# Performance work log

Measured on AMD Instinct MI355X. Metric: run time of the kernel, lower is better.

Reference implementation:

```python
import jax, jax.numpy as jnp
import numpy as np

WS = 7            # window size
HEADS = 4
DIM = 128         # hidden_dim
HEAD_DIM = 128    # wrapper passes head_dim=hidden_dim (faithful to source)
INNER = HEADS * HEAD_DIM   # 512
MLP = 4 * DIM
PATCH = 4
DISP = WS // 2
NEG = -1e9


def _ln(x, g, b, eps=1e-5):
    m = jnp.mean(x, -1, keepdims=True)
    v = jnp.mean((x - m) ** 2, -1, keepdims=True)
    return (x - m) * jax.lax.rsqrt(v + eps) * g + b


_coords = np.stack(np.meshgrid(np.arange(WS), np.arange(WS), indexing='ij'), -1).reshape(-1, 2)
REL_IDX = jnp.asarray(_coords[None] - _coords[:, None] + WS - 1)  # (ws^2, ws^2, 2)


def _build_masks():
    n = WS * WS
    ul = np.zeros((n, n), np.float32)
    ul[-DISP * WS:, : -DISP * WS] = NEG
    ul[: -DISP * WS, -DISP * WS:] = NEG
    lr = np.zeros((WS, WS, WS, WS), np.float32)
    lr[:, -DISP:, :, : -DISP] = NEG
    lr[:, : -DISP, :, -DISP:] = NEG
    return jnp.asarray(ul), jnp.asarray(lr.reshape(n, n))

UL_MASK, LR_MASK = _build_masks()


def _win_attn(x, w_qkv, pos, w_o, b_o, shifted):
    b, H, W, _ = x.shape
    if shifted:
        x = jnp.roll(x, (-DISP, -DISP), axis=(1, 2))
    nh, nw = H // WS, W // WS
    qkv = x @ w_qkv  # (b, H, W, 3*INNER)

    def to_win(t):  # -> (b, heads, n_windows, ws*ws, head_dim)
        t = t.reshape(b, nh, WS, nw, WS, HEADS, HEAD_DIM)
        return t.transpose(0, 5, 1, 3, 2, 4, 6).reshape(b, HEADS, nh * nw, WS * WS, HEAD_DIM)

    q, k, v = map(to_win, jnp.split(qkv, 3, axis=-1))
    dots = jnp.einsum('bhwid,bhwjd->bhwij', q, k) * (HEAD_DIM ** -0.5)
    dots = dots + pos[REL_IDX[..., 0], REL_IDX[..., 1]]  # shared across heads (berniwal)
    if shifted:
        dots = dots.at[:, :, -nw:].add(UL_MASK)
        dots = dots.at[:, :, nw - 1::nw].add(LR_MASK)
    attn = jax.nn.softmax(dots, axis=-1)
    out = jnp.einsum('bhwij,bhwjd->bhwid', attn, v)
    out = out.reshape(b, HEADS, nh, nw, WS, WS, HEAD_DIM).transpose(0, 2, 4, 3, 5, 1, 6)
    out = out.reshape(b, H, W, INNER) @ w_o + b_o
    if shifted:
        out = jnp.roll(out, (DISP, DISP), axis=(1, 2))
    return out


def _block(x, ga1, be1, w_qkv, pos, w_o, b_o, ga2, be2, w1, b1, w2, b2, shifted):
    x = x + _win_attn(_ln(x, ga1, be1), w_qkv, pos, w_o, b_o, shifted)
    h = jax.nn.gelu(_ln(x, ga2, be2) @ w1 + b1, approximate=False) @ w2 + b2
    return x + h


def _patch_embed(x, w, b):  # Unfold(patch) + Linear, channel-major feature order
    B, C, H, W = x.shape
    nh, nw = H // PATCH, W // PATCH
    x = x.reshape(B, C, nh, PATCH, nw, PATCH).transpose(0, 2, 4, 1, 3, 5)
    return x.reshape(B, nh, nw, C * PATCH * PATCH) @ w + b


def setup_inputs() -> dict:
    key = jax.random.key(0)
    ks = iter(jax.random.split(key, 48))

    def nrm(shape, s=0.02):
        return jax.random.normal(next(ks), shape, dtype=jnp.float32) * s

    inp = {'x': jax.random.normal(next(ks), (32, 3, 224, 224), dtype=jnp.float32)}
    inp['w_pe'] = nrm((3 * PATCH * PATCH, DIM))
    inp['b_pe'] = jnp.zeros((DIM,), jnp.float32)
    for s in ('a', 'b'):
        inp['ga1_' + s] = jnp.ones((DIM,), jnp.float32)
        inp['be1_' + s] = jnp.zeros((DIM,), jnp.float32)
        inp['w_qkv_' + s] = nrm((DIM, 3 * INNER))
        inp['pos_' + s] = nrm((2 * WS - 1, 2 * WS - 1), 1.0)
        inp['w_o_' + s] = nrm((INNER, DIM))
        inp['b_o_' + s] = jnp.zeros((DIM,), jnp.float32)
        inp['ga2_' + s] = jnp.ones((DIM,), jnp.float32)
        inp['be2_' + s] = jnp.zeros((DIM,), jnp.float32)
        inp['w_m1_' + s] = nrm((DIM, MLP))
        inp['b_m1_' + s] = jnp.zeros((MLP,), jnp.float32)
        inp['w_m2_' + s] = nrm((MLP, DIM))
        inp['b_m2_' + s] = jnp.zeros((DIM,), jnp.float32)
    return inp


def reference(x, w_pe, b_pe,
              ga1_a, be1_a, w_qkv_a, pos_a, w_o_a, b_o_a, ga2_a, be2_a, w_m1_a, b_m1_a, w_m2_a, b_m2_a,
              ga1_b, be1_b, w_qkv_b, pos_b, w_o_b, b_o_b, ga2_b, be2_b, w_m1_b, b_m1_b, w_m2_b, b_m2_b):
    h = _patch_embed(x, w_pe, b_pe)  # (B, 56, 56, DIM)
    h = _block(h, ga1_a, be1_a, w_qkv_a, pos_a, w_o_a, b_o_a, ga2_a, be2_a, w_m1_a, b_m1_a, w_m2_a, b_m2_a, False)
    h = _block(h, ga1_b, be1_b, w_qkv_b, pos_b, w_o_b, b_o_b, ga2_b, be2_b, w_m1_b, b_m1_b, w_m2_b, b_m2_b, True)
    return h
```

## Files before the change

### kernel.cpp

```cpp
#include <hip/hip_runtime.h>

typedef __attribute__((ext_vector_type(8))) short bf16x8;
typedef __attribute__((ext_vector_type(4))) short bf16x4;
typedef __attribute__((ext_vector_type(4))) float f32x4;
typedef __attribute__((ext_vector_type(2))) unsigned u32x2;

#define MFMA16(a, b, c) __builtin_amdgcn_mfma_f32_16x16x32_bf16(a, b, c, 0, 0, 0)

static __device__ __forceinline__ short f2bf(float f) {
    union { float f; unsigned u; } x; x.f = f;
    unsigned r = x.u + 0x7FFFu + ((x.u >> 16) & 1u);
    return (short)(r >> 16);
}

static __device__ __forceinline__ unsigned cvtpk(float lo, float hi) {
    unsigned r;
    asm("v_cvt_pk_bf16_f32 %0, %1, %2" : "=v"(r) : "v"(lo), "v"(hi));
    return r;
}

static __device__ __forceinline__ void gload16(const void* g, void* l) {
    __builtin_amdgcn_global_load_lds((const __attribute__((address_space(1))) void*)g,
                                     (__attribute__((address_space(3))) void*)l, 16, 0, 0);
}

static __device__ __forceinline__ float gelu(float t) {
    return 0.5f * t * (1.f + erff(t * 0.70710678118f));
}

__global__ void wconv_kernel(const float* __restrict__ i_qkv, const float* __restrict__ i_o,
                             const float* __restrict__ i_m1, const float* __restrict__ i_m2,
                             short* __restrict__ wqkv, short* __restrict__ wo,
                             short* __restrict__ wm1, short* __restrict__ wm2) {
    int idx = blockIdx.x * 256 + threadIdx.x;
    if (idx < 196608) {
        int k = idx & 127, n = idx >> 7;
        wqkv[idx] = f2bf(i_qkv[k * 1536 + n]);
    } else if (idx < 262144) {
        int l = idx - 196608; int k = l & 511, n = l >> 9;
        wo[l] = f2bf(i_o[k * 128 + n]);
    } else if (idx < 327680) {
        int l = idx - 262144; int k = l & 127, n = l >> 7;
        wm1[l] = f2bf(i_m1[k * 512 + n]);
    } else {
        int l = idx - 327680; int k = l & 511, n = l >> 9;
        wm2[l] = f2bf(i_m2[k * 128 + n]);
    }
}

__global__ void tabgen_kernel(const float* __restrict__ pos_a, const float* __restrict__ pos_b,
                              float* __restrict__ tab) {
    int v = blockIdx.x;
    const float* pos = (v == 0) ? pos_a : pos_b;
    for (int e = threadIdx.x; e < 4096; e += 256) {
        int row = e >> 6, key = e & 63;
        float val;
        if (key >= 49) val = -1e9f;
        else if (row >= 49) val = 0.f;
        else {
            int qi = row / 7, qj = row - qi * 7, ki = key / 7, kj = key - ki * 7;
            val = pos[(ki - qi + 6) * 13 + (kj - qj + 6)];
            if (v >= 1) {
                bool wh7 = (v - 1) & 2, ww7 = (v - 1) & 1;
                if (wh7 && ((qi >= 4) != (ki >= 4))) val += -1e9f;
                if (ww7 && ((qj >= 4) != (kj >= 4))) val += -1e9f;
            }
        }
        tab[v * 4096 + e] = val;
    }
}

__global__ __launch_bounds__(256) void patchln_kernel(const float* __restrict__ x,
                                                      const float* __restrict__ w,
                                                      const float* __restrict__ bias,
                                                      const float* __restrict__ g,
                                                      const float* __restrict__ bta,
                                                      float* __restrict__ out,
                                                      short* __restrict__ xn) {
    __shared__ float s_in[2][48];
    __shared__ float red[2][2][2];
    const int tid = threadIdx.x;
    const int half = tid >> 7, c = tid & 127;
    const int winh = (tid >> 6) & 1, lane = tid & 63;
    const int t = blockIdx.x * 2 + half;
    const int b = t / 3136, rem = t - b * 3136;
    const int hp = rem / 56, wp = rem - hp * 56;
    if (c < 48) {
        int cin = c >> 4, py = (c >> 2) & 3, px = c & 3;
        s_in[half][c] = x[((size_t)(b * 3 + cin) * 224 + hp * 4 + py) * 224 + wp * 4 + px];
    }
    __syncthreads();
    float acc = bias[c];
#pragma unroll
    for (int k = 0; k < 48; ++k) acc += s_in[half][k] * w[k * 128 + c];
    out[(size_t)t * 128 + c] = acc;
    float s1 = acc, s2 = acc * acc;
#pragma unroll
    for (int o = 32; o > 0; o >>= 1) { s1 += __shfl_xor(s1, o); s2 += __shfl_xor(s2, o); }
    if (lane == 0) { red[half][winh][0] = s1; red[half][winh][1] = s2; }
    __syncthreads();
    s1 = red[half][0][0] + red[half][1][0];
    s2 = red[half][0][1] + red[half][1][1];
    float mean = s1 * (1.f / 128.f);
    float var = s2 * (1.f / 128.f) - mean * mean;
    float rstd = rsqrtf(var + 1e-5f);
    xn[(size_t)t * 128 + c] = f2bf((acc - mean) * rstd * g[c] + bta[c]);
}

template <int SHIFTED>
__global__ __launch_bounds__(256, 3) void attn_kernel(const short* __restrict__ xn,
                                                      const short* __restrict__ wqkvT,
                                                      const float* __restrict__ tab,
                                                      const short* __restrict__ zpad,
                                                      short* __restrict__ aout) {
    __shared__ short smem[24576];
    short* s_x = smem;
    short* s_q = smem + 8192;
    short* s_k = smem + 16384;
    short* s_vT = smem + 8192;
    short* s_p = smem + 16384;

    const int tid = threadIdx.x;
    const int wid = tid >> 6, lane = tid & 63;
    const int l15 = lane & 15, l4 = lane >> 4, klo = l4 * 8;
    const int bid = blockIdx.x;
    const int win = bid & 63, head = (bid >> 6) & 3, b = bid >> 8;
    const int wh = win >> 3, ww = win & 7;

#pragma unroll
    for (int it = 0; it < 4; ++it) {
        int slot = it * 256 + tid;
        int row = slot >> 4, scol = slot & 15;
        int colb = (scol * 16) ^ ((row & 7) << 4);
        const char* g;
        if (row < 49) {
            int wi = (row * 37) >> 8, wj = row - wi * 7;
            int hh = wh * 7 + wi, wp = ww * 7 + wj;
            if (SHIFTED) { hh += 3; if (hh >= 56) hh -= 56; wp += 3; if (wp >= 56) wp -= 56; }
            int t = (b * 56 + hh) * 56 + wp;
            g = (const char*)(xn + (size_t)t * 128) + colb;
        } else {
            g = (const char*)zpad + colb;
        }
        gload16(g, (char*)smem + (it * 256 + wid * 64) * 16);
    }
    __syncthreads();

    const f32x4 zero4 = {0.f, 0.f, 0.f, 0.f};

    {
        const short* Wq = wqkvT + (size_t)(head * 128) * 128;
        const short* Wk = wqkvT + (size_t)(512 + head * 128) * 128;
        f32x4 aq[2][4], ak[2][4];
#pragma unroll
        for (int mw = 0; mw < 2; ++mw)
#pragma unroll
            for (int j = 0; j < 4; ++j) { aq[mw][j] = zero4; ak[mw][j] = zero4; }
#pragma unroll
        for (int k0 = 0; k0 < 4; ++k0) {
            bf16x8 bx[4], awq[2], awk[2];
#pragma unroll
            for (int j = 0; j < 4; ++j) {
                int row = j * 16 + l15;
                bx[j] = *(const bf16x8*)((const char*)s_x + row * 256 + ((k0 * 64 + l4 * 16) ^ ((row & 7) << 4)));
            }
#pragma unroll
            for (int mw = 0; mw < 2; ++mw) {
                awq[mw] = *(const bf16x8*)(Wq + (size_t)(wid * 32 + mw * 16 + l15) * 128 + k0 * 32 + klo);
                awk[mw] = *(const bf16x8*)(Wk + (size_t)(wid * 32 + mw * 16 + l15) * 128 + k0 * 32 + klo);
            }
            __builtin_amdgcn_s_setprio(1);
#pragma unroll
            for (int mw = 0; mw < 2; ++mw)
#pragma unroll
                for (int j = 0; j < 4; ++j) {
                    aq[mw][j] = MFMA16(awq[mw], bx[j], aq[mw][j]);
                    ak[mw][j] = MFMA16(awk[mw], bx[j], ak[mw][j]);
                }
            __builtin_amdgcn_s_setprio(0);
        }
#pragma unroll
        for (int mw = 0; mw < 2; ++mw)
#pragma unroll
            for (int j = 0; j < 4; ++j) {
                u32x2 pq = { cvtpk(aq[mw][j][0], aq[mw][j][1]), cvtpk(aq[mw][j][2], aq[mw][j][3]) };
                u32x2 pk = { cvtpk(ak[mw][j][0], ak[mw][j][1]), cvtpk(ak[mw][j][2], ak[mw][j][3]) };
                int row = j * 16 + l15;
                int colb = (wid * 64 + mw * 32 + l4 * 8) ^ ((row & 7) << 4);
                *(u32x2*)((char*)s_q + row * 256 + colb) = pq;
                *(u32x2*)((char*)s_k + row * 256 + colb) = pk;
            }
    }
    __syncthreads();

    const int qrow = wid * 16 + l15;
    f32x4 dt[4];
#pragma unroll
    for (int m = 0; m < 4; ++m) dt[m] = zero4;
#pragma unroll
    for (int k0 = 0; k0 < 4; ++k0) {
        bf16x8 bq = *(const bf16x8*)((const char*)s_q + qrow * 256 + ((k0 * 64 + l4 * 16) ^ ((qrow & 7) << 4)));
        __builtin_amdgcn_s_setprio(1);
#pragma unroll
        for (int m = 0; m < 4; ++m) {
            int krow = m * 16 + l15;
            bf16x8 akf = *(const bf16x8*)((const char*)s_k + krow * 256 + ((k0 * 64 + l4 * 16) ^ ((krow & 7) << 4)));
            dt[m] = MFMA16(akf, bq, dt[m]);
        }
        __builtin_amdgcn_s_setprio(0);
    }
    __syncthreads();

    const int variant = SHIFTED ? (1 + ((wh == 7) ? 2 : 0) + ((ww == 7) ? 1 : 0)) : 0;
    const float* tv = tab + variant * 4096 + qrow * 64;
    const float SC = 0.08838834764831845f;
    float p[4][4];
    float mx = -3.0e38f;
#pragma unroll
    for (int m = 0; m < 4; ++m) {
        f32x4 tb = *(const f32x4*)(tv + m * 16 + l4 * 4);
#pragma unroll
        for (int r = 0; r < 4; ++r) {
            float d = dt[m][r] * SC + tb[r];
            p[m][r] = d;
            mx = fmaxf(mx, d);
        }
    }
    mx = fmaxf(mx, __shfl_xor(mx, 16));
    mx = fmaxf(mx, __shfl_xor(mx, 32));
    float sum = 0.f;
#pragma unroll
    for (int m = 0; m < 4; ++m)
#pragma unroll
        for (int r = 0; r < 4; ++r) { p[m][r] = __expf(p[m][r] - mx); sum += p[m][r]; }
    sum += __shfl_xor(sum, 16);
    sum += __shfl_xor(sum, 32);
    float inv = 1.f / sum;
#pragma unroll
    for (int m = 0; m < 4; ++m) {
        u32x2 pv = { cvtpk(p[m][0] * inv, p[m][1] * inv), cvtpk(p[m][2] * inv, p[m][3] * inv) };
        *(u32x2*)((char*)s_p + qrow * 128 + ((m * 32 + l4 * 8) ^ ((qrow & 7) << 4))) = pv;
    }

    {
        const short* Wv = wqkvT + (size_t)(1024 + head * 128) * 128;
        f32x4 acc[4][2];
#pragma unroll
        for (int m = 0; m < 4; ++m)
#pragma unroll
            for (int n = 0; n < 2; ++n) acc[m][n] = zero4;
#pragma unroll
        for (int k0 = 0; k0 < 4; ++k0) {
            bf16x8 ax[4], bw[2];
#pragma unroll
            for (int m = 0; m < 4; ++m) {
                int row = m * 16 + l15;
                ax[m] = *(const bf16x8*)((const char*)s_x + row * 256 + ((k0 * 64 + l4 * 16) ^ ((row & 7) << 4)));
            }
#pragma unroll
            for (int n = 0; n < 2; ++n)
                bw[n] = *(const bf16x8*)(Wv + (size_t)(wid * 32 + n * 16 + l15) * 128 + k0 * 32 + klo);
            __builtin_amdgcn_s_setprio(1);
#pragma unroll
            for (int m = 0; m < 4; ++m)
#pragma unroll
                for (int n = 0; n < 2; ++n) acc[m][n] = MFMA16(ax[m], bw[n], acc[m][n]);
            __builtin_amdgcn_s_setprio(0);
        }
#pragma unroll
        for (int m = 0; m < 4; ++m)
#pragma unroll
            for (int n = 0; n < 2; ++n) {
                u32x2 pv = { cvtpk(acc[m][n][0], acc[m][n][1]), cvtpk(acc[m][n][2], acc[m][n][3]) };
                int hd = wid * 32 + n * 16 + l15;
                *(u32x2*)((char*)s_vT + hd * 128 + ((m * 32 + l4 * 8) ^ ((hd & 7) << 4))) = pv;
            }
    }
    __syncthreads();

    f32x4 o[4][2];
#pragma unroll
    for (int m = 0; m < 4; ++m)
#pragma unroll
        for (int n = 0; n < 2; ++n) o[m][n] = zero4;
#pragma unroll
    for (int k0 = 0; k0 < 2; ++k0) {
        bf16x8 ap[4], bv[2];
#pragma unroll
        for (int m = 0; m < 4; ++m) {
            int row = m * 16 + l15;
            ap[m] = *(const bf16x8*)((const char*)s_p + row * 128 + ((k0 * 64 + l4 * 16) ^ ((row & 7) << 4)));
        }
#pragma unroll
        for (int n = 0; n < 2; ++n) {
            int hd = wid * 32 + n * 16 + l15;
            bv[n] = *(const bf16x8*)((const char*)s_vT + hd * 128 + ((k0 * 64 + l4 * 16) ^ ((hd & 7) << 4)));
        }
        __builtin_amdgcn_s_setprio(1);
#pragma unroll
        for (int m = 0; m < 4; ++m)
#pragma unroll
            for (int n = 0; n < 2; ++n) o[m][n] = MFMA16(ap[m], bv[n], o[m][n]);
        __builtin_amdgcn_s_setprio(0);
    }
#pragma unroll
    for (int m = 0; m < 4; ++m) {
#pragma unroll
        for (int r = 0; r < 4; ++r) {
            int rl = m * 16 + l4 * 4 + r;
            if (rl < 49) {
                int wi = (rl * 37) >> 8, wj = rl - wi * 7;
                int hh = wh * 7 + wi, wp = ww * 7 + wj;
                if (SHIFTED) { hh += 3; if (hh >= 56) hh -= 56; wp += 3; if (wp >= 56) wp -= 56; }
                size_t t = (size_t)(b * 56 + hh) * 56 + wp;
                aout[t * 512 + head * 128 + wid * 32 + l15] = f2bf(o[m][0][r]);
                aout[t * 512 + head * 128 + wid * 32 + 16 + l15] = f2bf(o[m][1][r]);
            }
        }
    }
}

__global__ __launch_bounds__(256, 2) void projmlp_kernel(const short* __restrict__ A,
                                                         const short* __restrict__ woT,
                                                         const short* __restrict__ wm1T,
                                                         const float* __restrict__ b_o,
                                                         const float* __restrict__ ga2,
                                                         const float* __restrict__ be2,
                                                         const float* __restrict__ b1,
                                                         float* __restrict__ outf,
                                                         short* __restrict__ hid) {
    __shared__ char smem[65536];
    float* red = (float*)(smem + 32768);

    const int tid = threadIdx.x, wid = tid >> 6, lane = tid & 63;
    const int wr = wid >> 1, wc = wid & 1;
    const int l15 = lane & 15, l4 = lane >> 4;
    const int m0 = blockIdx.x * 128;

    auto stage = [&](int kc, int bi) {
#pragma unroll
        for (int it = 0; it < 4; ++it) {
            int slot = it * 256 + tid;
            int row = slot >> 3, scol = slot & 7;
            int colb = (scol * 16) ^ ((row & 7) << 4);
            gload16((const char*)(A + (size_t)(m0 + row) * 512 + kc * 64) + colb,
                    (char*)smem + bi * 32768 + (it * 256 + wid * 64) * 16);
        }
#pragma unroll
        for (int it = 0; it < 4; ++it) {
            int slot = it * 256 + tid;
            int row = slot >> 3, scol = slot & 7;
            int colb = (scol * 16) ^ ((row & 7) << 4);
            gload16((const char*)(woT + (size_t)row * 512 + kc * 64) + colb,
                    (char*)smem + bi * 32768 + 16384 + (it * 256 + wid * 64) * 16);
        }
    };

    const f32x4 zero4 = {0.f, 0.f, 0.f, 0.f};
    f32x4 acc[4][4];
#pragma unroll
    for (int nf = 0; nf < 4; ++nf)
#pragma unroll
        for (int tm = 0; tm < 4; ++tm) acc[nf][tm] = zero4;

    stage(0, 0);
    __syncthreads();
#pragma unroll
    for (int kc = 0; kc < 8; ++kc) {
        if (kc + 1 < 8) stage(kc + 1, (kc + 1) & 1);
        const char* bufA = (const char*)smem + (kc & 1) * 32768;
        const char* bufB = bufA + 16384;
#pragma unroll
        for (int ks = 0; ks < 2; ++ks) {
            bf16x8 a[4], bfr[4];
#pragma unroll
            for (int tm = 0; tm < 4; ++tm) {
                int row = wr * 64 + tm * 16 + l15;
                a[tm] = *(const bf16x8*)(bufA + row * 128 + ((ks * 64 + l4 * 16) ^ ((row & 7) << 4)));
            }
#pragma unroll
            for (int nf = 0; nf < 4; ++nf) {
                int row = wc * 64 + nf * 16 + l15;
                bfr[nf] = *(const bf16x8*)(bufB + row * 128 + ((ks * 64 + l4 * 16) ^ ((row & 7) << 4)));
            }
            __builtin_amdgcn_s_setprio(1);
#pragma unroll
            for (int nf = 0; nf < 4; ++nf)
#pragma unroll
                for (int tm = 0; tm < 4; ++tm) acc[nf][tm] = MFMA16(bfr[nf], a[tm], acc[nf][tm]);
            __builtin_amdgcn_s_setprio(0);
        }
        __syncthreads();
    }

    f32x4 bv4[4];
#pragma unroll
    for (int nf = 0; nf < 4; ++nf)
        bv4[nf] = *(const f32x4*)(b_o + wc * 64 + nf * 16 + l4 * 4);

    float s1[4], s2[4];
#pragma unroll
    for (int tm = 0; tm < 4; ++tm) {
        int row = m0 + wr * 64 + tm * 16 + l15;
        float a1 = 0.f, a2 = 0.f;
#pragma unroll
        for (int nf = 0; nf < 4; ++nf) {
            f32x4 rs = *(const f32x4*)(outf + (size_t)row * 128 + wc * 64 + nf * 16 + l4 * 4);
#pragma unroll
            for (int r = 0; r < 4; ++r) {
                float v = acc[nf][tm][r] + bv4[nf][r] + rs[r];
                acc[nf][tm][r] = v;
                a1 += v; a2 += v * v;
            }
        }
        s1[tm] = a1; s2[tm] = a2;
    }
#pragma unroll
    for (int tm = 0; tm < 4; ++tm) {
        s1[tm] += __shfl_xor(s1[tm], 16); s1[tm] += __shfl_xor(s1[tm], 32);
        s2[tm] += __shfl_xor(s2[tm], 16); s2[tm] += __shfl_xor(s2[tm], 32);
    }
    if (l4 == 0) {
#pragma unroll
        for (int tm = 0; tm < 4; ++tm) {
            int lrow = wr * 64 + tm * 16 + l15;
            red[lrow * 4 + wc * 2] = s1[tm];
            red[lrow * 4 + wc * 2 + 1] = s2[tm];
        }
    }
    __syncthreads();

    float mean[4], rstd[4];
#pragma unroll
    for (int tm = 0; tm < 4; ++tm) {
        int lrow = wr * 64 + tm * 16 + l15;
        f32x4 rd = *(const f32x4*)(red + lrow * 4);
        float t1 = rd[0] + rd[2], t2 = rd[1] + rd[3];
        mean[tm] = t1 * (1.f / 128.f);
        float var = t2 * (1.f / 128.f) - mean[tm] * mean[tm];
        rstd[tm] = rsqrtf(var + 1e-5f);
    }
    __syncthreads();

#pragma unroll
    for (int tm = 0; tm < 4; ++tm) {
        int lrow = wr * 64 + tm * 16 + l15;
        int row = m0 + lrow;
#pragma unroll
        for (int nf = 0; nf < 4; ++nf) {
            int col0 = wc * 64 + nf * 16 + l4 * 4;
            *(f32x4*)(outf + (size_t)row * 128 + col0) = acc[nf][tm];
            f32x4 gg = *(const f32x4*)(ga2 + col0);
            f32x4 bb = *(const f32x4*)(be2 + col0);
            float w0 = (acc[nf][tm][0] - mean[tm]) * rstd[tm] * gg[0] + bb[0];
            float w1 = (acc[nf][tm][1] - mean[tm]) * rstd[tm] * gg[1] + bb[1];
            float w2 = (acc[nf][tm][2] - mean[tm]) * rstd[tm] * gg[2] + bb[2];
            float w3 = (acc[nf][tm][3] - mean[tm]) * rstd[tm] * gg[3] + bb[3];
            u32x2 pb = { cvtpk(w0, w1), cvtpk(w2, w3) };
            *(u32x2*)((char*)smem + lrow * 256 + ((col0 * 2) ^ ((lrow & 7) << 4))) = pb;
        }
    }
    __syncthreads();

    for (int hc = 0; hc < 4; ++hc) {
#pragma unroll
        for (int it = 0; it < 8; ++it) {
            int slot = it * 256 + tid;
            int row = slot >> 4, scol = slot & 15;
            int colb = (scol * 16) ^ ((row & 7) << 4);
            gload16((const char*)(wm1T + (size_t)(hc * 128 + row) * 128) + colb,
                    (char*)smem + 32768 + (it * 256 + wid * 64) * 16);
        }
        __syncthreads();

#pragma unroll
        for (int nf = 0; nf < 4; ++nf)
#pragma unroll
            for (int tm = 0; tm < 4; ++tm) acc[nf][tm] = zero4;
#pragma unroll
        for (int ks = 0; ks < 4; ++ks) {
            bf16x8 a[4], bfr[4];
#pragma unroll
            for (int tm = 0; tm < 4; ++tm) {
                int row = wr * 64 + tm * 16 + l15;
                a[tm] = *(const bf16x8*)((const char*)smem + row * 256 + ((ks * 64 + l4 * 16) ^ ((row & 7) << 4)));
            }
#pragma unroll
            for (int nf = 0; nf < 4; ++nf) {
                int hrow = wc * 64 + nf * 16 + l15;
                bfr[nf] = *(const bf16x8*)((const char*)smem + 32768 + hrow * 256 + ((ks * 64 + l4 * 16) ^ ((hrow & 7) << 4)));
            }
            __builtin_amdgcn_s_setprio(1);
#pragma unroll
            for (int nf = 0; nf < 4; ++nf)
#pragma unroll
                for (int tm = 0; tm < 4; ++tm) acc[nf][tm] = MFMA16(bfr[nf], a[tm], acc[nf][tm]);
            __builtin_amdgcn_s_setprio(0);
        }

        f32x4 b14[4];
#pragma unroll
        for (int nf = 0; nf < 4; ++nf)
            b14[nf] = *(const f32x4*)(b1 + hc * 128 + wc * 64 + nf * 16 + l4 * 4);
#pragma unroll
        for (int tm = 0; tm < 4; ++tm) {
            int row = m0 + wr * 64 + tm * 16 + l15;
#pragma unroll
            for (int nf = 0; nf < 4; ++nf) {
                float v0 = gelu(acc[nf][tm][0] + b14[nf][0]);
                float v1 = gelu(acc[nf][tm][1] + b14[nf][1]);
                float v2 = gelu(acc[nf][tm][2] + b14[nf][2]);
                float v3 = gelu(acc[nf][tm][3] + b14[nf][3]);
                u32x2 pv = { cvtpk(v0, v1), cvtpk(v2, v3) };
                *(u32x2*)(hid + (size_t)row * 512 + hc * 128 + wc * 64 + nf * 16 + l4 * 4) = pv;
            }
        }
        __syncthreads();
    }
}

template <int MODE>
__global__ __launch_bounds__(256, 2) void gemm4_kernel(const short* __restrict__ A,
                                                       const short* __restrict__ BT,
                                                       const float* __restrict__ bias,
                                                       const float* __restrict__ g,
                                                       const float* __restrict__ bta,
                                                       float* __restrict__ outf,
                                                       short* __restrict__ outb) {
    __shared__ char smem[65536];
    float* red = (float*)smem;

    const int tid = threadIdx.x, wid = tid >> 6, lane = tid & 63;
    const int wr = wid >> 1, wc = wid & 1;
    const int l15 = lane & 15, l4 = lane >> 4;
    const int m0 = blockIdx.x * 128;

    auto stage = [&](int kc, int bi) {
#pragma unroll
        for (int it = 0; it < 4; ++it) {
            int slot = it * 256 + tid;
            int row = slot >> 3, scol = slot & 7;
            int colb = (scol * 16) ^ ((row & 7) << 4);
            gload16((const char*)(A + (size_t)(m0 + row) * 512 + kc * 64) + colb,
                    (char*)smem + bi * 32768 + (it * 256 + wid * 64) * 16);
        }
#pragma unroll
        for (int it = 0; it < 4; ++it) {
            int slot = it * 256 + tid;
            int row = slot >> 3, scol = slot & 7;
            int colb = (scol * 16) ^ ((row & 7) << 4);
            gload16((const char*)(BT + (size_t)row * 512 + kc * 64) + colb,
                    (char*)smem + bi * 32768 + 16384 + (it * 256 + wid * 64) * 16);
        }
    };

    const f32x4 zero4 = {0.f, 0.f, 0.f, 0.f};
    f32x4 acc[4][4];
#pragma unroll
    for (int nf = 0; nf < 4; ++nf)
#pragma unroll
        for (int tm = 0; tm < 4; ++tm) acc[nf][tm] = zero4;

    stage(0, 0);
    __syncthreads();
#pragma unroll
    for (int kc = 0; kc < 8; ++kc) {
        if (kc + 1 < 8) stage(kc + 1, (kc + 1) & 1);
        const char* bufA = (const char*)smem + (kc & 1) * 32768;
        const char* bufB = bufA + 16384;
#pragma unroll
        for (int ks = 0; ks < 2; ++ks) {
            bf16x8 a[4], bfr[4];
#pragma unroll
            for (int tm = 0; tm < 4; ++tm) {
                int row = wr * 64 + tm * 16 + l15;
                a[tm] = *(const bf16x8*)(bufA + row * 128 + ((ks * 64 + l4 * 16) ^ ((row & 7) << 4)));
            }
#pragma unroll
            for (int nf = 0; nf < 4; ++nf) {
                int row = wc * 64 + nf * 16 + l15;
                bfr[nf] = *(const bf16x8*)(bufB + row * 128 + ((ks * 64 + l4 * 16) ^ ((row & 7) << 4)));
            }
            __builtin_amdgcn_s_setprio(1);
#pragma unroll
            for (int nf = 0; nf < 4; ++nf)
#pragma unroll
                for (int tm = 0; tm < 4; ++tm) acc[nf][tm] = MFMA16(bfr[nf], a[tm], acc[nf][tm]);
            __builtin_amdgcn_s_setprio(0);
        }
        __syncthreads();
    }

    f32x4 bv4[4];
#pragma unroll
    for (int nf = 0; nf < 4; ++nf)
        bv4[nf] = *(const f32x4*)(bias + wc * 64 + nf * 16 + l4 * 4);

    float s1[4], s2[4];
#pragma unroll
    for (int tm = 0; tm < 4; ++tm) {
        int row = m0 + wr * 64 + tm * 16 + l15;
        float a1 = 0.f, a2 = 0.f;
#pragma unroll
        for (int nf = 0; nf < 4; ++nf) {
            f32x4 rs = *(const f32x4*)(outf + (size_t)row * 128 + wc * 64 + nf * 16 + l4 * 4);
#pragma unroll
            for (int r = 0; r < 4; ++r) {
                float v = acc[nf][tm][r] + bv4[nf][r] + rs[r];
                acc[nf][tm][r] = v;
                a1 += v; a2 += v * v;
            }
        }
        s1[tm] = a1; s2[tm] = a2;
    }

    if (MODE == 1) {
#pragma unroll
        for (int tm = 0; tm < 4; ++tm) {
            s1[tm] += __shfl_xor(s1[tm], 16); s1[tm] += __shfl_xor(s1[tm], 32);
            s2[tm] += __shfl_xor(s2[tm], 16); s2[tm] += __shfl_xor(s2[tm], 32);
        }
        if (l4 == 0) {
#pragma unroll
            for (int tm = 0; tm < 4; ++tm) {
                int lrow = wr * 64 + tm * 16 + l15;
                red[lrow * 4 + wc * 2] = s1[tm];
                red[lrow * 4 + wc * 2 + 1] = s2[tm];
            }
        }
        __syncthreads();
    }

#pragma unroll
    for (int tm = 0; tm < 4; ++tm) {
        int lrow = wr * 64 + tm * 16 + l15;
        int row = m0 + lrow;
        float mean = 0.f, rstd = 0.f;
        if (MODE == 1) {
            f32x4 rd = *(const f32x4*)(red + lrow * 4);
            float t1 = rd[0] + rd[2], t2 = rd[1] + rd[3];
            mean = t1 * (1.f / 128.f);
            float var = t2 * (1.f / 128.f) - mean * mean;
            rstd = rsqrtf(var + 1e-5f);
        }
#pragma unroll
        for (int nf = 0; nf < 4; ++nf) {
            int col0 = wc * 64 + nf * 16 + l4 * 4;
            *(f32x4*)(outf + (size_t)row * 128 + col0) = acc[nf][tm];
            if (MODE == 1) {
                f32x4 gg = *(const f32x4*)(g + col0);
                f32x4 bb = *(const f32x4*)(bta + col0);
                float w0 = (acc[nf][tm][0] - mean) * rstd * gg[0] + bb[0];
                float w1 = (acc[nf][tm][1] - mean) * rstd * gg[1] + bb[1];
                float w2 = (acc[nf][tm][2] - mean) * rstd * gg[2] + bb[2];
                float w3 = (acc[nf][tm][3] - mean) * rstd * gg[3] + bb[3];
                u32x2 pb = { cvtpk(w0, w1), cvtpk(w2, w3) };
                *(u32x2*)(outb + (size_t)row * 128 + col0) = pb;
            }
        }
    }
}

extern "C" void kernel_launch(void* const* d_in, const int* in_sizes, int n_in,
                              void* d_out, int out_size, void* d_ws, size_t ws_size,
                              hipStream_t stream) {
    const float* x = (const float*)d_in[0];
    const float* w_pe = (const float*)d_in[1];
    const float* b_pe = (const float*)d_in[2];
    const float* P[24];
    for (int i = 0; i < 24; ++i) P[i] = (const float*)d_in[3 + i];

    float* out = (float*)d_out;
    const size_t TOK = 100352;

    short* xn = (short*)d_ws;
    short* abuf = xn + TOK * 128;
    short* wqkv = abuf + TOK * 512;
    short* wo = wqkv + 196608;
    short* wm1 = wo + 65536;
    short* wm2 = wm1 + 65536;
    float* tab = (float*)(wm2 + 65536);
    short* zpad = (short*)(tab + 5 * 4096);

    hipMemsetAsync(zpad, 0, 256, stream);
    tabgen_kernel<<<5, 256, 0, stream>>>(P[3], P[15], tab);

    patchln_kernel<<<50176, 256, 0, stream>>>(x, w_pe, b_pe, P[0], P[1], out, xn);

    for (int s = 0; s < 2; ++s) {
        wconv_kernel<<<1536, 256, 0, stream>>>(P[s * 12 + 2], P[s * 12 + 4], P[s * 12 + 8], P[s * 12 + 10],
                                               wqkv, wo, wm1, wm2);

        if (s == 0)
            attn_kernel<0><<<8192, 256, 0, stream>>>(xn, wqkv, tab, zpad, abuf);
        else
            attn_kernel<1><<<8192, 256, 0, stream>>>(xn, wqkv, tab, zpad, abuf);

        projmlp_kernel<<<784, 256, 0, stream>>>(
            abuf, wo, wm1, P[s * 12 + 5], P[s * 12 + 6], P[s * 12 + 7], P[s * 12 + 9], out, abuf);

        if (s == 0)
            gemm4_kernel<1><<<784, 256, 0, stream>>>(
                abuf, wm2, P[11], P[12], P[13], out, xn);
        else
            gemm4_kernel<2><<<784, 256, 0, stream>>>(
                abuf, wm2, P[23], nullptr, nullptr, out, nullptr);
    }
}
```

Measured before the change: 594.3 us.

## Fold Wq·Wkᵀ into a per-head matrix so attention skips the K projection

A new per-head 128x128 matrix M = Wq_h·Wk_hᵀ·scale is precomputed from the weights in fp32 and stored in bf16. The attention kernel now computes T = X·M and forms the scores as T·Xᵀ directly against the staged input, so it no longer projects K and no longer applies the scale per element. The V projection moves into the first GEMM phase alongside T, which removes one staged-input pass, and the shared-memory regions are reassigned. The cost is a small extra weight-precompute kernel per block, plus different rounding because M is formed in fp32 but stored in bf16. The MLP accumulator is renamed, which may affect register allocation.

```diff
diff --git a/kernel.cpp b/kernel.cpp
--- a/kernel.cpp
+++ b/kernel.cpp
@@ -46,6 +46,20 @@
         int l = idx - 327680; int k = l & 511, n = l >> 9;
         wm2[l] = f2bf(i_m2[k * 128 + n]);
     }
+}
+
+__global__ __launch_bounds__(128) void mtgen_kernel(const float* __restrict__ wqkv,
+                                                    short* __restrict__ mt) {
+    const int h = blockIdx.x >> 7, e = blockIdx.x & 127;
+    __shared__ float s_wk[128];
+    const int d = threadIdx.x;
+    s_wk[d] = wqkv[(size_t)e * 1536 + 512 + h * 128 + d];
+    __syncthreads();
+    const float* wq = wqkv + (size_t)d * 1536 + h * 128;
+    float acc = 0.f;
+#pragma unroll
+    for (int o = 0; o < 128; ++o) acc += wq[o] * s_wk[o];
+    mt[(size_t)(h * 128 + e) * 128 + d] = f2bf(acc * 0.08838834764831845f);
 }
 
 __global__ void tabgen_kernel(const float* __restrict__ pos_a, const float* __restrict__ pos_b,
@@ -110,15 +124,15 @@
 template <int SHIFTED>
 __global__ __launch_bounds__(256, 3) void attn_kernel(const short* __restrict__ xn,
                                                       const short* __restrict__ wqkvT,
+                                                      const short* __restrict__ mt,
                                                       const float* __restrict__ tab,
                                                       const short* __restrict__ zpad,
                                                       short* __restrict__ aout) {
     __shared__ short smem[24576];
     short* s_x = smem;
-    short* s_q = smem + 8192;
-    short* s_k = smem + 16384;
-    short* s_vT = smem + 8192;
-    short* s_p = smem + 16384;
+    short* s_T = smem + 8192;
+    short* s_v = smem + 16384;
+    short* s_p = smem;
 
     const int tid = threadIdx.x;
     const int wid = tid >> 6, lane = tid & 63;
@@ -149,46 +163,57 @@
     const f32x4 zero4 = {0.f, 0.f, 0.f, 0.f};
 
     {
-        const short* Wq = wqkvT + (size_t)(head * 128) * 128;
-        const short* Wk = wqkvT + (size_t)(512 + head * 128) * 128;
-        f32x4 aq[2][4], ak[2][4];
+        const short* Mh = mt + (size_t)head * 16384;
+        const short* Wv = wqkvT + (size_t)(1024 + head * 128) * 128;
+        f32x4 at[2][4], av[4][2];
 #pragma unroll
         for (int mw = 0; mw < 2; ++mw)
 #pragma unroll
-            for (int j = 0; j < 4; ++j) { aq[mw][j] = zero4; ak[mw][j] = zero4; }
+            for (int j = 0; j < 4; ++j) at[mw][j] = zero4;
+#pragma unroll
+        for (int m = 0; m < 4; ++m)
+#pragma unroll
+            for (int n = 0; n < 2; ++n) av[m][n] = zero4;
 #pragma unroll
         for (int k0 = 0; k0 < 4; ++k0) {
-            bf16x8 bx[4], awq[2], awk[2];
+            bf16x8 bx[4], awt[2], bwv[2];
 #pragma unroll
             for (int j = 0; j < 4; ++j) {
                 int row = j * 16 + l15;
                 bx[j] = *(const bf16x8*)((const char*)s_x + row * 256 + ((k0 * 64 + l4 * 16) ^ ((row & 7) << 4)));
             }
 #pragma unroll
-            for (int mw = 0; mw < 2; ++mw) {
-                awq[mw] = *(const bf16x8*)(Wq + (size_t)(wid * 32 + mw * 16 + l15) * 128 + k0 * 32 + klo);
-                awk[mw] = *(const bf16x8*)(Wk + (size_t)(wid * 32 + mw * 16 + l15) * 128 + k0 * 32 + klo);
-            }
+            for (int mw = 0; mw < 2; ++mw)
+                awt[mw] = *(const bf16x8*)(Mh + (size_t)(wid * 32 + mw * 16 + l15) * 128 + k0 * 32 + klo);
+#pragma unroll
+            for (int n = 0; n < 2; ++n)
+                bwv[n] = *(const bf16x8*)(Wv + (size_t)(wid * 32 + n * 16 + l15) * 128 + k0 * 32 + klo);
             __builtin_amdgcn_s_setprio(1);
 #pragma unroll
             for (int mw = 0; mw < 2; ++mw)
 #pragma unroll
-                for (int j = 0; j < 4; ++j) {
-                    aq[mw][j] = MFMA16(awq[mw], bx[j], aq[mw][j]);
-                    ak[mw][j] = MFMA16(awk[mw], bx[j], ak[mw][j]);
-                }
+                for (int j = 0; j < 4; ++j) at[mw][j] = MFMA16(awt[mw], bx[j], at[mw][j]);
+#pragma unroll
+            for (int m = 0; m < 4; ++m)
+#pragma unroll
+                for (int n = 0; n < 2; ++n) av[m][n] = MFMA16(bx[m], bwv[n], av[m][n]);
             __builtin_amdgcn_s_setprio(0);
         }
 #pragma unroll
         for (int mw = 0; mw < 2; ++mw)
 #pragma unroll
             for (int j = 0; j < 4; ++j) {
-                u32x2 pq = { cvtpk(aq[mw][j][0], aq[mw][j][1]), cvtpk(aq[mw][j][2], aq[mw][j][3]) };
-                u32x2 pk = { cvtpk(ak[mw][j][0], ak[mw][j][1]), cvtpk(ak[mw][j][2], ak[mw][j][3]) };
+                u32x2 pq = { cvtpk(at[mw][j][0], at[mw][j][1]), cvtpk(at[mw][j][2], at[mw][j][3]) };
                 int row = j * 16 + l15;
-                int colb = (wid * 64 + mw * 32 + l4 * 8) ^ ((row & 7) << 4);
-                *(u32x2*)((char*)s_q + row * 256 + colb) = pq;
-                *(u32x2*)((char*)s_k + row * 256 + colb) = pk;
+                *(u32x2*)((char*)s_T + row * 256 + ((wid * 64 + mw * 32 + l4 * 8) ^ ((row & 7) << 4))) = pq;
+            }
+#pragma unroll
+        for (int m = 0; m < 4; ++m)
+#pragma unroll
+            for (int n = 0; n < 2; ++n) {
+                u32x2 pv = { cvtpk(av[m][n][0], av[m][n][1]), cvtpk(av[m][n][2], av[m][n][3]) };
+                int hd = wid * 32 + n * 16 + l15;
+                *(u32x2*)((char*)s_v + hd * 128 + ((m * 32 + l4 * 8) ^ ((hd & 7) << 4))) = pv;
             }
     }
     __syncthreads();
@@ -199,12 +224,12 @@
     for (int m = 0; m < 4; ++m) dt[m] = zero4;
 #pragma unroll
     for (int k0 = 0; k0 < 4; ++k0) {
-        bf16x8 bq = *(const bf16x8*)((const char*)s_q + qrow * 256 + ((k0 * 64 + l4 * 16) ^ ((qrow & 7) << 4)));
+        bf16x8 bq = *(const bf16x8*)((const char*)s_T + qrow * 256 + ((k0 * 64 + l4 * 16) ^ ((qrow & 7) << 4)));
         __builtin_amdgcn_s_setprio(1);
 #pragma unroll
         for (int m = 0; m < 4; ++m) {
             int krow = m * 16 + l15;
-            bf16x8 akf = *(const bf16x8*)((const char*)s_k + krow * 256 + ((k0 * 64 + l4 * 16) ^ ((krow & 7) << 4)));
+            bf16x8 akf = *(const bf16x8*)((const char*)s_x + krow * 256 + ((k0 * 64 + l4 * 16) ^ ((krow & 7) << 4)));
             dt[m] = MFMA16(akf, bq, dt[m]);
         }
         __builtin_amdgcn_s_setprio(0);
@@ -213,7 +238,6 @@
 
     const int variant = SHIFTED ? (1 + ((wh == 7) ? 2 : 0) + ((ww == 7) ? 1 : 0)) : 0;
     const float* tv = tab + variant * 4096 + qrow * 64;
-    const float SC = 0.08838834764831845f;
     float p[4][4];
     float mx = -3.0e38f;
 #pragma unroll
@@ -221,7 +245,7 @@
         f32x4 tb = *(const f32x4*)(tv + m * 16 + l4 * 4);
 #pragma unroll
         for (int r = 0; r < 4; ++r) {
-            float d = dt[m][r] * SC + tb[r];
+            float d = dt[m][r] + tb[r];
             p[m][r] = d;
             mx = fmaxf(mx, d);
         }
@@ -241,41 +265,6 @@
         u32x2 pv = { cvtpk(p[m][0] * inv, p[m][1] * inv), cvtpk(p[m][2] * inv, p[m][3] * inv) };
         *(u32x2*)((char*)s_p + qrow * 128 + ((m * 32 + l4 * 8) ^ ((qrow & 7) << 4))) = pv;
     }
-
-    {
-        const short* Wv = wqkvT + (size_t)(1024 + head * 128) * 128;
-        f32x4 acc[4][2];
-#pragma unroll
-        for (int m = 0; m < 4; ++m)
-#pragma unroll
-            for (int n = 0; n < 2; ++n) acc[m][n] = zero4;
-#pragma unroll
-        for (int k0 = 0; k0 < 4; ++k0) {
-            bf16x8 ax[4], bw[2];
-#pragma unroll
-            for (int m = 0; m < 4; ++m) {
-                int row = m * 16 + l15;
-                ax[m] = *(const bf16x8*)((const char*)s_x + row * 256 + ((k0 * 64 + l4 * 16) ^ ((row & 7) << 4)));
-            }
-#pragma unroll
-            for (int n = 0; n < 2; ++n)
-                bw[n] = *(const bf16x8*)(Wv + (size_t)(wid * 32 + n * 16 + l15) * 128 + k0 * 32 + klo);
-            __builtin_amdgcn_s_setprio(1);
-#pragma unroll
-            for (int m = 0; m < 4; ++m)
-#pragma unroll
-                for (int n = 0; n < 2; ++n) acc[m][n] = MFMA16(ax[m], bw[n], acc[m][n]);
-            __builtin_amdgcn_s_setprio(0);
-        }
-#pragma unroll
-        for (int m = 0; m < 4; ++m)
-#pragma unroll
-            for (int n = 0; n < 2; ++n) {
-                u32x2 pv = { cvtpk(acc[m][n][0], acc[m][n][1]), cvtpk(acc[m][n][2], acc[m][n][3]) };
-                int hd = wid * 32 + n * 16 + l15;
-                *(u32x2*)((char*)s_vT + hd * 128 + ((m * 32 + l4 * 8) ^ ((hd & 7) << 4))) = pv;
-            }
-    }
     __syncthreads();
 
     f32x4 o[4][2];
@@ -294,7 +283,7 @@
 #pragma unroll
         for (int n = 0; n < 2; ++n) {
             int hd = wid * 32 + n * 16 + l15;
-            bv[n] = *(const bf16x8*)((const char*)s_vT + hd * 128 + ((k0 * 64 + l4 * 16) ^ ((hd & 7) << 4)));
+            bv[n] = *(const bf16x8*)((const char*)s_v + hd * 128 + ((k0 * 64 + l4 * 16) ^ ((hd & 7) << 4)));
         }
         __builtin_amdgcn_s_setprio(1);
 #pragma unroll
@@ -473,10 +462,11 @@
         }
         __syncthreads();
 
+        f32x4 acc2[4][4];
 #pragma unroll
         for (int nf = 0; nf < 4; ++nf)
 #pragma unroll
-            for (int tm = 0; tm < 4; ++tm) acc[nf][tm] = zero4;
+            for (int tm = 0; tm < 4; ++tm) acc2[nf][tm] = zero4;
 #pragma unroll
         for (int ks = 0; ks < 4; ++ks) {
             bf16x8 a[4], bfr[4];
@@ -494,7 +484,7 @@
 #pragma unroll
             for (int nf = 0; nf < 4; ++nf)
 #pragma unroll
-                for (int tm = 0; tm < 4; ++tm) acc[nf][tm] = MFMA16(bfr[nf], a[tm], acc[nf][tm]);
+                for (int tm = 0; tm < 4; ++tm) acc2[nf][tm] = MFMA16(bfr[nf], a[tm], acc2[nf][tm]);
             __builtin_amdgcn_s_setprio(0);
         }
 
@@ -507,10 +497,10 @@
             int row = m0 + wr * 64 + tm * 16 + l15;
 #pragma unroll
             for (int nf = 0; nf < 4; ++nf) {
-                float v0 = gelu(acc[nf][tm][0] + b14[nf][0]);
-                float v1 = gelu(acc[nf][tm][1] + b14[nf][1]);
-                float v2 = gelu(acc[nf][tm][2] + b14[nf][2]);
-                float v3 = gelu(acc[nf][tm][3] + b14[nf][3]);
+                float v0 = gelu(acc2[nf][tm][0] + b14[nf][0]);
+                float v1 = gelu(acc2[nf][tm][1] + b14[nf][1]);
+                float v2 = gelu(acc2[nf][tm][2] + b14[nf][2]);
+                float v3 = gelu(acc2[nf][tm][3] + b14[nf][3]);
                 u32x2 pv = { cvtpk(v0, v1), cvtpk(v2, v3) };
                 *(u32x2*)(hid + (size_t)row * 512 + hc * 128 + wc * 64 + nf * 16 + l4 * 4) = pv;
             }
@@ -679,7 +669,8 @@
     short* wo = wqkv + 196608;
     short* wm1 = wo + 65536;
     short* wm2 = wm1 + 65536;
-    float* tab = (float*)(wm2 + 65536);
+    short* mtb = wm2 + 65536;
+    float* tab = (float*)(mtb + 65536);
     short* zpad = (short*)(tab + 5 * 4096);
 
     hipMemsetAsync(zpad, 0, 256, stream);
@@ -690,11 +681,12 @@
     for (int s = 0; s < 2; ++s) {
         wconv_kernel<<<1536, 256, 0, stream>>>(P[s * 12 + 2], P[s * 12 + 4], P[s * 12 + 8], P[s * 12 + 10],
                                                wqkv, wo, wm1, wm2);
+        mtgen_kernel<<<512, 128, 0, stream>>>(P[s * 12 + 2], mtb);
 
         if (s == 0)
-            attn_kernel<0><<<8192, 256, 0, stream>>>(xn, wqkv, tab, zpad, abuf);
+            attn_kernel<0><<<8192, 256, 0, stream>>>(xn, wqkv, mtb, tab, zpad, abuf);
         else
-            attn_kernel<1><<<8192, 256, 0, stream>>>(xn, wqkv, tab, zpad, abuf);
+            attn_kernel<1><<<8192, 256, 0, stream>>>(xn, wqkv, mtb, tab, zpad, abuf);
 
         projmlp_kernel<<<784, 256, 0, stream>>>(
             abuf, wo, wm1, P[s * 12 + 5], P[s * 12 + 6], P[s * 12 + 7], P[s * 12 + 9], out, abuf);
```

New measurement: 549.9 us, median of 3. 7.5% less time.
